# Kernel optimization log

Hardware: AMD Instinct MI355X
Metric: run time of the kernel (lower is better)

## Reference

```python
import jax, jax.numpy as jnp
import numpy as np

SQRT2 = np.float32(np.sqrt(2.0))
D = 256


def setup_inputs() -> dict:
    key = jax.random.key(0)
    k1, = jax.random.split(key, 1)
    x = jax.random.normal(k1, (4, 1024, D), dtype=jnp.float32)
    weight = jnp.ones((D,), dtype=jnp.float32)
    bias = jnp.zeros((D,), dtype=jnp.float32)
    return {"x": x, "weight": weight, "bias": bias}


def reference(x, weight, bias):
    orig_shape = x.shape
    d = orig_shape[-1]
    flat = x.reshape(-1, d)  # [N, D]
    # Silverman 2d bandwidth: 0.9 * std(ddof=1, dim=-1) * D^(-1/5)
    bw = 0.9 * jnp.std(flat, axis=-1, ddof=1) * np.float32(d ** (-0.2))  # [N]
    # Pairwise Gaussian-kernel CDF, averaged over data points (dim 2).
    scaled = (flat[:, :, None] - flat[:, None, :]) / bw[:, None, None]  # [N, D, D]
    cdf = jnp.mean(0.5 * (1.0 + jax.lax.erf(scaled / SQRT2)), axis=2)  # [N, D]
    # Gaussian PPF (inverse CDF)
    normed = jax.lax.erf_inv(2.0 * cdf - 1.0) * SQRT2  # [N, D]
    out = normed.reshape(orig_shape) * weight + bias
    return out
```

## Files before the change

kernel.cpp:

```cpp
#include <hip/hip_runtime.h>
#include <math.h>

#define DD 256
#define NW 4
#define MFREQ 60
#define LPER 84.0f

typedef float v2f __attribute__((ext_vector_type(2)));

template <int CTRL>
__device__ __forceinline__ float dpp_add(float x) {
    return x + __int_as_float(__builtin_amdgcn_update_dpp(
        0, __float_as_int(x), CTRL, 0xf, 0xf, false));
}
__device__ __forceinline__ float wave_sum(float x) {
    x = dpp_add<0x111>(x);
    x = dpp_add<0x112>(x);
    x = dpp_add<0x114>(x);
    x = dpp_add<0x118>(x);
    x = dpp_add<0x142>(x);
    x = dpp_add<0x143>(x);
    return __int_as_float(__builtin_amdgcn_readlane(__float_as_int(x), 63));
}

__global__ __launch_bounds__(64 * NW, 4) void kd_layernorm_kernel(
        const float* __restrict__ x,
        const float* __restrict__ w,
        const float* __restrict__ bia,
        float* __restrict__ out) {
    const int lane = threadIdx.x & 63;
    const int wid  = threadIdx.x >> 6;
    const int row  = blockIdx.x * NW + wid;
    const float* xr = x + (size_t)row * DD;

    float u0 = xr[lane], u1 = xr[64 + lane], u2 = xr[128 + lane], u3 = xr[192 + lane];

    float ssum = wave_sum((u0 + u1) + (u2 + u3));
    float qsum = wave_sum(__builtin_fmaf(u0, u0, u1 * u1) +
                          __builtin_fmaf(u2, u2, u3 * u3));
    float var = (qsum - ssum * ssum * (1.0f / DD)) * (1.0f / (DD - 1));
    float bw = 0.9f * __builtin_sqrtf(var) * 0.32987697769322355f;
    float scale = 1.0f / bw;
    float v0 = u0 * scale, v1 = u1 * scale, v2 = u2 * scale, v3 = u3 * scale;
    float meanv = ssum * scale * (1.0f / DD);

    const float w1 = 6.28318530717958648f / LPER;
    v2f s1a = {__sinf(w1 * v0), __sinf(w1 * v1)};
    v2f s1b = {__sinf(w1 * v2), __sinf(w1 * v3)};
    v2f c1a = {__cosf(w1 * v0), __cosf(w1 * v1)};
    v2f c1b = {__cosf(w1 * v2), __cosf(w1 * v3)};

    v2f sma = s1a, smb = s1b, cma = c1a, cmb = c1b;
    v2f Ra = {0.f, 0.f}, Rb = {0.f, 0.f};

    float g   = __expf(-0.5f * w1 * w1);
    float rr  = __expf(-1.5f * w1 * w1);
    const float rho = __expf(-w1 * w1);
    float fm = 1.0f;

    #pragma clang loop unroll_count(1)
    for (int m = 1; m <= MFREQ; ++m) {
        v2f sp = sma + smb;
        v2f cp = cma + cmb;
        float Stot = wave_sum(sp.x + sp.y);
        float Ctot = wave_sum(cp.x + cp.y);
        float sc = g * 0.31830988618f * __builtin_amdgcn_rcpf(fm);
        float gC = Ctot * sc, gS = Stot * sc;
        v2f vgC = {gC, gC}, vgS = {gS, gS};
        Ra = __builtin_elementwise_fma(sma, vgC, Ra);
        Ra = __builtin_elementwise_fma(cma, -vgS, Ra);
        Rb = __builtin_elementwise_fma(smb, vgC, Rb);
        Rb = __builtin_elementwise_fma(cmb, -vgS, Rb);
        v2f nsa = __builtin_elementwise_fma(sma, c1a, cma * s1a);
        v2f nca = __builtin_elementwise_fma(cma, c1a, -(sma * s1a));
        v2f nsb = __builtin_elementwise_fma(smb, c1b, cmb * s1b);
        v2f ncb = __builtin_elementwise_fma(cmb, c1b, -(smb * s1b));
        sma = nsa; cma = nca; smb = nsb; cmb = ncb;
        g *= rr; rr *= rho; fm += 1.0f;
    }

    float vv[4] = {v0, v1, v2, v3};
    float Rv[4] = {Ra.x, Ra.y, Rb.x, Rb.y};
    #pragma unroll
    for (int a = 0; a < 4; ++a) {
        float y = 2.0f * ((vv[a] - meanv) * (1.0f / LPER) + Rv[a] * (1.0f / DD));
        float normed = erfinvf(y) * 1.41421356237309505f;
        int idx = a * 64 + lane;
        out[(size_t)row * DD + idx] = __builtin_fmaf(normed, w[idx], bia[idx]);
    }
}

extern "C" void kernel_launch(void* const* d_in, const int* in_sizes, int n_in,
                              void* d_out, int out_size, void* d_ws, size_t ws_size,
                              hipStream_t stream) {
    const float* x = (const float*)d_in[0];
    const float* w = (const float*)d_in[1];
    const float* b = (const float*)d_in[2];
    float* out = (float*)d_out;
    const int nrows = in_sizes[0] / DD;
    kd_layernorm_kernel<<<nrows / NW, 64 * NW, 0, stream>>>(x, w, b, out);
}
```

Measured before the change: 80.37 us.

## Adapt Fourier period and term count per row, use cheap erfinv polynomial

Each row's Fourier series period is now derived from its own data range, found with wave-wide max/min reductions. The number of harmonics M is set per row from that period, capped at 96, instead of a fixed 60. This is meant to cut loop iterations for rows with a narrow range. The library erfinvf is replaced by a single-branch Giles polynomial, and the hardware sin, cos, exp2 and rcp intrinsics are used. The single-branch polynomial loses accuracy near the tails, and rows with a wide range may now run more iterations than before.

After: 67.56 us. 1.19x faster.

```diff
diff --git a/kernel.cpp b/kernel.cpp
--- a/kernel.cpp
+++ b/kernel.cpp
@@ -3,8 +3,6 @@
 
 #define DD 256
 #define NW 4
-#define MFREQ 60
-#define LPER 84.0f
 
 typedef float v2f __attribute__((ext_vector_type(2)));
 
@@ -13,19 +11,54 @@
     return x + __int_as_float(__builtin_amdgcn_update_dpp(
         0, __float_as_int(x), CTRL, 0xf, 0xf, false));
 }
+template <int CTRL>
+__device__ __forceinline__ float dpp_mov_self(float x) {
+    return __int_as_float(__builtin_amdgcn_update_dpp(
+        __float_as_int(x), __float_as_int(x), CTRL, 0xf, 0xf, false));
+}
 __device__ __forceinline__ float wave_sum(float x) {
-    x = dpp_add<0x111>(x);
-    x = dpp_add<0x112>(x);
-    x = dpp_add<0x114>(x);
-    x = dpp_add<0x118>(x);
-    x = dpp_add<0x142>(x);
-    x = dpp_add<0x143>(x);
+    x = dpp_add<0x111>(x); x = dpp_add<0x112>(x);
+    x = dpp_add<0x114>(x); x = dpp_add<0x118>(x);
+    x = dpp_add<0x142>(x); x = dpp_add<0x143>(x);
     return __int_as_float(__builtin_amdgcn_readlane(__float_as_int(x), 63));
+}
+__device__ __forceinline__ float wave_max(float x) {
+    x = __builtin_fmaxf(x, dpp_mov_self<0x111>(x));
+    x = __builtin_fmaxf(x, dpp_mov_self<0x112>(x));
+    x = __builtin_fmaxf(x, dpp_mov_self<0x114>(x));
+    x = __builtin_fmaxf(x, dpp_mov_self<0x118>(x));
+    x = __builtin_fmaxf(x, dpp_mov_self<0x142>(x));
+    x = __builtin_fmaxf(x, dpp_mov_self<0x143>(x));
+    return __int_as_float(__builtin_amdgcn_readlane(__float_as_int(x), 63));
+}
+__device__ __forceinline__ float wave_min(float x) {
+    x = __builtin_fminf(x, dpp_mov_self<0x111>(x));
+    x = __builtin_fminf(x, dpp_mov_self<0x112>(x));
+    x = __builtin_fminf(x, dpp_mov_self<0x114>(x));
+    x = __builtin_fminf(x, dpp_mov_self<0x118>(x));
+    x = __builtin_fminf(x, dpp_mov_self<0x142>(x));
+    x = __builtin_fminf(x, dpp_mov_self<0x143>(x));
+    return __int_as_float(__builtin_amdgcn_readlane(__float_as_int(x), 63));
+}
+
+__device__ __forceinline__ float ppf_from_y(float y) {
+    float omy2 = __builtin_fmaf(-y, y, 1.0f);
+    float wg = __builtin_fmaf(-__builtin_amdgcn_logf(omy2), 0.69314718056f, -2.5f);
+    float p = 2.81022636e-08f;
+    p = __builtin_fmaf(p, wg, 3.43273939e-07f);
+    p = __builtin_fmaf(p, wg, -3.5233877e-06f);
+    p = __builtin_fmaf(p, wg, -4.39150654e-06f);
+    p = __builtin_fmaf(p, wg, 0.00021858087f);
+    p = __builtin_fmaf(p, wg, -0.00125372503f);
+    p = __builtin_fmaf(p, wg, -0.00417768164f);
+    p = __builtin_fmaf(p, wg, 0.246640727f);
+    p = __builtin_fmaf(p, wg, 1.50140941f);
+    return p * y * 1.41421356237309505f;
 }
 
 __global__ __launch_bounds__(64 * NW, 4) void kd_layernorm_kernel(
         const float* __restrict__ x,
-        const float* __restrict__ w,
+        const float* __restrict__ wgt,
         const float* __restrict__ bia,
         float* __restrict__ out) {
     const int lane = threadIdx.x & 63;
@@ -38,28 +71,39 @@
     float ssum = wave_sum((u0 + u1) + (u2 + u3));
     float qsum = wave_sum(__builtin_fmaf(u0, u0, u1 * u1) +
                           __builtin_fmaf(u2, u2, u3 * u3));
+    float xmax = wave_max(__builtin_fmaxf(__builtin_fmaxf(u0, u1),
+                                          __builtin_fmaxf(u2, u3)));
+    float xmin = wave_min(__builtin_fminf(__builtin_fminf(u0, u1),
+                                          __builtin_fminf(u2, u3)));
+
     float var = (qsum - ssum * ssum * (1.0f / DD)) * (1.0f / (DD - 1));
     float bw = 0.9f * __builtin_sqrtf(var) * 0.32987697769322355f;
-    float scale = 1.0f / bw;
-    float v0 = u0 * scale, v1 = u1 * scale, v2 = u2 * scale, v3 = u3 * scale;
-    float meanv = ssum * scale * (1.0f / DD);
+    float invbw = __builtin_amdgcn_rcpf(bw);
+    float v0 = u0 * invbw, v1 = u1 * invbw, v2 = u2 * invbw, v3 = u3 * invbw;
+    float meanv = ssum * invbw * (1.0f / DD);
 
-    const float w1 = 6.28318530717958648f / LPER;
-    v2f s1a = {__sinf(w1 * v0), __sinf(w1 * v1)};
-    v2f s1b = {__sinf(w1 * v2), __sinf(w1 * v3)};
-    v2f c1a = {__cosf(w1 * v0), __cosf(w1 * v1)};
-    v2f c1b = {__cosf(w1 * v2), __cosf(w1 * v3)};
+    float L = (xmax - xmin) * invbw + 10.0f;
+    float invL = __builtin_amdgcn_rcpf(L);
+    int M = (int)__builtin_ceilf(0.70028175f * L);
+    M = M < 1 ? 1 : (M > 96 ? 96 : M);
+    M = __builtin_amdgcn_readfirstlane(M);
+
+    v2f s1a = {__builtin_amdgcn_sinf(v0 * invL), __builtin_amdgcn_sinf(v1 * invL)};
+    v2f s1b = {__builtin_amdgcn_sinf(v2 * invL), __builtin_amdgcn_sinf(v3 * invL)};
+    v2f c1a = {__builtin_amdgcn_cosf(v0 * invL), __builtin_amdgcn_cosf(v1 * invL)};
+    v2f c1b = {__builtin_amdgcn_cosf(v2 * invL), __builtin_amdgcn_cosf(v3 * invL)};
 
     v2f sma = s1a, smb = s1b, cma = c1a, cmb = c1b;
     v2f Ra = {0.f, 0.f}, Rb = {0.f, 0.f};
 
-    float g   = __expf(-0.5f * w1 * w1);
-    float rr  = __expf(-1.5f * w1 * w1);
-    const float rho = __expf(-w1 * w1);
+    float w1sq = 39.4784176044f * invL * invL;
+    float g   = __builtin_amdgcn_exp2f(-0.72134752f * w1sq);
+    float rr  = __builtin_amdgcn_exp2f(-2.16404256f * w1sq);
+    const float rho = __builtin_amdgcn_exp2f(-1.44269504f * w1sq);
     float fm = 1.0f;
 
     #pragma clang loop unroll_count(1)
-    for (int m = 1; m <= MFREQ; ++m) {
+    for (int m = 1; m <= M; ++m) {
         v2f sp = sma + smb;
         v2f cp = cma + cmb;
         float Stot = wave_sum(sp.x + sp.y);
@@ -83,10 +127,10 @@
     float Rv[4] = {Ra.x, Ra.y, Rb.x, Rb.y};
     #pragma unroll
     for (int a = 0; a < 4; ++a) {
-        float y = 2.0f * ((vv[a] - meanv) * (1.0f / LPER) + Rv[a] * (1.0f / DD));
-        float normed = erfinvf(y) * 1.41421356237309505f;
+        float y = 2.0f * __builtin_fmaf(vv[a] - meanv, invL, Rv[a] * (1.0f / DD));
+        float normed = ppf_from_y(y);
         int idx = a * 64 + lane;
-        out[(size_t)row * DD + idx] = __builtin_fmaf(normed, w[idx], bia[idx]);
+        out[(size_t)row * DD + idx] = __builtin_fmaf(normed, wgt[idx], bia[idx]);
     }
 }
 
```
